# Kernel tuning notes

Hardware: AMD Instinct MI355X
Metric: run time of the kernel (lower is better)

## Reference

```python
import jax, jax.numpy as jnp
import numpy as np

EPS = 1e-6  # T5LayerNorm epsilon


def setup_inputs() -> dict:
    key = jax.random.key(0)
    k0, k1, k2, k3 = jax.random.split(key, 4)
    B, S, D, F, E = 4, 2048, 768, 3072, 8
    hidden_states = jax.random.normal(k0, (B, S, D), jnp.float32)
    router_w = jax.random.normal(k1, (E, D), jnp.float32) * 0.02
    ln_w = jnp.ones((E, D), jnp.float32)
    wi = jax.random.normal(k2, (E, F, D), jnp.float32) * 0.02
    wo = jax.random.normal(k3, (E, D, F), jnp.float32) * 0.02
    return {"hidden_states": hidden_states, "router_w": router_w, "ln_w": ln_w,
            "wi": wi, "wo": wo, "top_k": 2}


def reference(hidden_states, router_w, ln_w, wi, wo, top_k):
    B, S, D = hidden_states.shape
    E = router_w.shape[0]
    x = hidden_states.reshape(-1, D)                      # [T, D] tokens
    router_logits = x @ router_w.T                        # [T, E]
    probs = jax.nn.softmax(router_logits, axis=-1)
    rw, sel = jax.lax.top_k(probs, top_k)                 # [T, K]
    rw = rw / jnp.sum(rw, axis=-1, keepdims=True)         # renormalize top-k weights

    # T5LayerNorm is RMS-norm (no mean subtraction); shared input x, per-expert scale.
    var = jnp.mean(x * x, axis=-1, keepdims=True)         # [T, 1]
    x_norm = x * jax.lax.rsqrt(var + EPS)                 # [T, D]

    out = jnp.zeros_like(x)
    for e in range(E):  # fixed small loop over experts (structurally distinct params)
        # combine weight for expert e: zero for tokens that did not select it
        w_e = jnp.sum(jnp.where(sel == e, rw, 0.0), axis=-1)   # [T]
        h = x_norm * ln_w[e]                                   # [T, D]
        ff = jax.nn.relu(h @ wi[e].T) @ wo[e].T                # [T, D]
        # T5LayerFF returns x + FFN(LN(x)); routing weight scales the whole output
        out = out + w_e[:, None] * (x + ff)
    layer_output = out.reshape(B, S, D)
    return layer_output, router_logits
```

## Files before the change

kernel.cpp:

```cpp
#include <hip/hip_runtime.h>
#include <hip/hip_bf16.h>
#include <math.h>

typedef short short8 __attribute__((ext_vector_type(8)));
typedef float f32x16 __attribute__((ext_vector_type(16)));

constexpr int D = 768;
constexpr int E = 8;
constexpr int F = 3072;
constexpr int FH = 1536;
constexpr int T = 8192;
constexpr float EPS = 1e-6f;

static __device__ inline unsigned short f2bf(float f) {
    __hip_bfloat16 h = __float2bfloat16(f);
    return *reinterpret_cast<unsigned short*>(&h);
}

static __device__ inline f32x16 mfma_bf16(short8 a, short8 b, f32x16 c) {
    return __builtin_amdgcn_mfma_f32_32x32x16_bf16(a, b, c, 0, 0, 0);
}

#define GLL16(g, s) __builtin_amdgcn_global_load_lds( \
    (const __attribute__((address_space(1))) unsigned int*)(g), \
    (__attribute__((address_space(3))) unsigned int*)(s), 16, 0, 0)

__global__ __launch_bounds__(256)
void convert_weights(const float* __restrict__ wi, const float* __restrict__ wo,
                     const float* __restrict__ lnw,
                     unsigned short* __restrict__ wip, unsigned short* __restrict__ wop)
{
    const unsigned NWI = (unsigned)E * F * D;
    unsigned i4 = (blockIdx.x * 256u + threadIdx.x) * 4u;
    if (i4 < NWI) {
        float4 v = *(const float4*)(wi + i4);
        unsigned e = i4 / (unsigned)(F * D);
        unsigned d = i4 % (unsigned)D;
        float4 l = *(const float4*)(lnw + e * D + d);
        ushort4 o = { f2bf(v.x * l.x), f2bf(v.y * l.y), f2bf(v.z * l.z), f2bf(v.w * l.w) };
        *(ushort4*)(wip + i4) = o;
    } else {
        unsigned j = i4 - NWI;
        float4 v = *(const float4*)(wo + j);
        ushort4 o = { f2bf(v.x), f2bf(v.y), f2bf(v.z), f2bf(v.w) };
        *(ushort4*)(wop + j) = o;
    }
}

__global__ __launch_bounds__(256)
void router_norm_kernel(const float* __restrict__ x,
                        const float* __restrict__ rw,
                        float* __restrict__ logits,
                        unsigned short* __restrict__ xn,
                        float* __restrict__ out,
                        int*   __restrict__ sel,
                        float2* __restrict__ w01)
{
    const int lane = threadIdx.x & 63;
    const int wid  = threadIdx.x >> 6;
    const int t = blockIdx.x * 4 + wid;
    if (t >= T) return;

    const float* xr = x + (size_t)t * D;
    float xv[12];
    float acc[8];
#pragma unroll
    for (int e = 0; e < 8; ++e) acc[e] = 0.f;
    float ssq = 0.f;
#pragma unroll
    for (int i = 0; i < 12; ++i) {
        const int k = lane + 64 * i;
        const float v = xr[k];
        xv[i] = v;
        ssq += v * v;
#pragma unroll
        for (int e = 0; e < 8; ++e) acc[e] += v * rw[e * D + k];
    }
#pragma unroll
    for (int off = 32; off; off >>= 1) {
        ssq += __shfl_xor(ssq, off);
#pragma unroll
        for (int e = 0; e < 8; ++e) acc[e] += __shfl_xor(acc[e], off);
    }

    int e0 = 0; float m0 = acc[0];
#pragma unroll
    for (int e = 1; e < 8; ++e) if (acc[e] > m0) { m0 = acc[e]; e0 = e; }
    int e1 = -1; float m1 = -3.4e38f;
#pragma unroll
    for (int e = 0; e < 8; ++e) if (e != e0 && acc[e] > m1) { m1 = acc[e]; e1 = e; }

    const float r  = expf(m1 - m0);
    const float w0 = 1.f / (1.f + r);
    const float w1 = r * w0;
    const float wsum = w0 + w1;
    const float rs = rsqrtf(ssq * (1.f / (float)D) + EPS);

    if (lane == 0) {
#pragma unroll
        for (int e = 0; e < 8; ++e) logits[t * 8 + e] = acc[e];
        sel[t] = e0 | (e1 << 4);
        w01[t] = make_float2(w0, w1);
    }

#pragma unroll
    for (int i = 0; i < 12; ++i) {
        const int k = lane + 64 * i;
        xn[(size_t)t * D + k] = f2bf(xv[i] * rs);
        out[(size_t)t * D + k] = wsum * xv[i];
    }
}

__global__ __launch_bounds__(256)
void build_lists(const int* __restrict__ sel, const float2* __restrict__ w01,
                 int* __restrict__ counts, int* __restrict__ lists,
                 float* __restrict__ wlist)
{
    const int e = blockIdx.x;
    const int tid = threadIdx.x;
    const int lane = tid & 63;
    const int wv = tid >> 6;
    __shared__ int wtot[4];
    int cnt = 0;
    for (int c0 = 0; c0 < T; c0 += 256) {
        const int t = c0 + tid;
        const int s = sel[t];
        const bool m1 = ((s >> 4) & 15) == e;
        const bool m = ((s & 15) == e) || m1;
        const unsigned long long b = __ballot(m);
        const int pre = __popcll(b & ((1ULL << lane) - 1ULL));
        if (lane == 0) wtot[wv] = __popcll(b);
        __syncthreads();
        int wbase = 0;
#pragma unroll
        for (int i = 0; i < 4; ++i) if (i < wv) wbase += wtot[i];
        if (m) {
            const int pos = cnt + wbase + pre;
            lists[e * T + pos] = (t << 1) | (m1 ? 1 : 0);
            const float2 w = w01[t];
            wlist[e * T + pos] = m1 ? w.y : w.x;
        }
        cnt += wtot[0] + wtot[1] + wtot[2] + wtot[3];
        __syncthreads();
    }
    if (tid == 0) counts[e] = cnt;
}

__global__ __launch_bounds__(256)
void gemm1_kernel(const unsigned short* __restrict__ xn,
                  const unsigned short* __restrict__ wip,
                  const int* __restrict__ counts,
                  const int* __restrict__ lists,
                  unsigned short* __restrict__ H, int half)
{
    __shared__ __align__(16) char smem[65536];
    __shared__ int s_tok[128];

    const int bid = blockIdx.x;
    const int e  = bid & 7;
    const int mt = (bid >> 3) / 12;
    const int nt = (bid >> 3) % 12;
    const int cnt = counts[e];
    const int base = mt * 128;
    if (base >= cnt) return;
    int offe = 0;
    for (int i = 0; i < e; ++i) offe += counts[i];

    const int tid = threadIdx.x;
    const int w = tid >> 6, l = tid & 63;
    const int lo = l & 31, hi = l >> 5;
    const int wr = w >> 1, wc = w & 1;

    if (tid < 128) {
        const int idx = base + tid;
        s_tok[tid] = (idx < cnt) ? (lists[e * T + idx] >> 1) : 0;
    }
    __syncthreads();

    const int r = (w * 4 + 0) * 8 + (l >> 3);
    const int chS = ((l & 7) ^ ((l >> 3) & 7)) * 8;
    const unsigned short* aSrc[4];
    const unsigned short* bSrc[4];
#pragma unroll
    for (int j = 0; j < 4; ++j) {
        const int rj = r + j * 8;
        aSrc[j] = xn + (size_t)s_tok[rj] * D + chS;
        bSrc[j] = wip + ((size_t)e * F + half * FH + nt * 128 + rj) * D + chS;
    }

    f32x16 acc00, acc01, acc10, acc11;
#pragma unroll
    for (int q = 0; q < 16; ++q) { acc00[q] = 0.f; acc01[q] = 0.f; acc10[q] = 0.f; acc11[q] = 0.f; }

    const int rx = (lo & 7) << 4;
    const int arow0 = (wr * 64 + lo) * 128;
    const int arow1 = arow0 + 32 * 128;
    const int brow0 = (wc * 64 + lo) * 128;
    const int brow1 = brow0 + 32 * 128;
    const int stgOff = w * 4096;

#pragma unroll
    for (int j = 0; j < 4; ++j) {
        GLL16(aSrc[j], smem + stgOff + j * 1024);
        GLL16(bSrc[j], smem + 16384 + stgOff + j * 1024);
    }
    __syncthreads();

    int cur = 0;
    for (int kt = 0; kt < 12; ++kt) {
        const char* bufA = smem + (cur ^ 1) * 32768;
        if (kt < 11) {
            const int k1 = (kt + 1) * 64;
#pragma unroll
            for (int j = 0; j < 4; ++j) {
                GLL16(aSrc[j] + k1, bufA + stgOff + j * 1024);
                GLL16(bSrc[j] + k1, bufA + 16384 + stgOff + j * 1024);
            }
        }
        const char* cA = smem + cur * 32768;
        const char* cB = cA + 16384;
#pragma unroll
        for (int ks = 0; ks < 4; ++ks) {
            const int coff = (hi * 16 + ks * 32) ^ rx;
            short8 a0 = *(const short8*)(cA + arow0 + coff);
            short8 a1 = *(const short8*)(cA + arow1 + coff);
            short8 b0 = *(const short8*)(cB + brow0 + coff);
            short8 b1 = *(const short8*)(cB + brow1 + coff);
            acc00 = mfma_bf16(a0, b0, acc00);
            acc01 = mfma_bf16(a0, b1, acc01);
            acc10 = mfma_bf16(a1, b0, acc10);
            acc11 = mfma_bf16(a1, b1, acc11);
        }
        __syncthreads();
        cur ^= 1;
    }

    const int cbase = nt * 128 + wc * 64 + lo;
#pragma unroll
    for (int rr = 0; rr < 16; ++rr) {
        const int crow = (rr & 3) + 8 * (rr >> 2) + 4 * hi;
        int lrow = wr * 64 + crow;
        if (base + lrow < cnt) {
            unsigned short* hp = H + (size_t)(offe + base + lrow) * FH + cbase;
            hp[0]  = f2bf(fmaxf(acc00[rr], 0.f));
            hp[32] = f2bf(fmaxf(acc01[rr], 0.f));
        }
        lrow += 32;
        if (base + lrow < cnt) {
            unsigned short* hp = H + (size_t)(offe + base + lrow) * FH + cbase;
            hp[0]  = f2bf(fmaxf(acc10[rr], 0.f));
            hp[32] = f2bf(fmaxf(acc11[rr], 0.f));
        }
    }
}

__global__ __launch_bounds__(256)
void gemm2_kernel(const unsigned short* __restrict__ H,
                  const unsigned short* __restrict__ wop,
                  const int* __restrict__ counts,
                  const int* __restrict__ lists, const float* __restrict__ wlist,
                  float* __restrict__ out, int half)
{
    __shared__ __align__(16) char smem[65536];
    __shared__ int   s_tok[128];
    __shared__ float s_wgt[128];

    const int bid = blockIdx.x;
    const int e  = bid & 7;
    const int mt = (bid >> 3) / 6;
    const int nt = (bid >> 3) % 6;
    const int cnt = counts[e];
    const int base = mt * 128;
    if (base >= cnt) return;
    int offe = 0;
    for (int i = 0; i < e; ++i) offe += counts[i];

    const int tid = threadIdx.x;
    const int w = tid >> 6, l = tid & 63;
    const int lo = l & 31, hi = l >> 5;
    const int wr = w >> 1, wc = w & 1;

    if (tid < 128) {
        const int idx = base + tid;
        const bool v = idx < cnt;
        s_tok[tid] = v ? lists[e * T + idx] : 0;
        s_wgt[tid] = v ? wlist[e * T + idx] : 0.f;
    }

    const int r = (w * 4 + 0) * 8 + (l >> 3);
    const int chS = ((l & 7) ^ ((l >> 3) & 7)) * 8;
    const unsigned short* aSrc[4];
    const unsigned short* bSrc[4];
#pragma unroll
    for (int j = 0; j < 4; ++j) {
        const int rj = r + j * 8;
        aSrc[j] = H + (size_t)(offe + base + rj) * FH + chS;
        bSrc[j] = wop + ((size_t)e * D + nt * 128 + rj) * F + half * FH + chS;
    }

    f32x16 acc00, acc01, acc10, acc11;
#pragma unroll
    for (int q = 0; q < 16; ++q) { acc00[q] = 0.f; acc01[q] = 0.f; acc10[q] = 0.f; acc11[q] = 0.f; }

    const int rx = (lo & 7) << 4;
    const int arow0 = (wr * 64 + lo) * 128;
    const int arow1 = arow0 + 32 * 128;
    const int brow0 = (wc * 64 + lo) * 128;
    const int brow1 = brow0 + 32 * 128;
    const int stgOff = w * 4096;

#pragma unroll
    for (int j = 0; j < 4; ++j) {
        GLL16(aSrc[j], smem + stgOff + j * 1024);
        GLL16(bSrc[j], smem + 16384 + stgOff + j * 1024);
    }
    __syncthreads();

    int cur = 0;
    for (int kt = 0; kt < 24; ++kt) {
        const char* bufA = smem + (cur ^ 1) * 32768;
        if (kt < 23) {
            const int k1 = (kt + 1) * 64;
#pragma unroll
            for (int j = 0; j < 4; ++j) {
                GLL16(aSrc[j] + k1, bufA + stgOff + j * 1024);
                GLL16(bSrc[j] + k1, bufA + 16384 + stgOff + j * 1024);
            }
        }
        const char* cA = smem + cur * 32768;
        const char* cB = cA + 16384;
#pragma unroll
        for (int ks = 0; ks < 4; ++ks) {
            const int coff = (hi * 16 + ks * 32) ^ rx;
            short8 a0 = *(const short8*)(cA + arow0 + coff);
            short8 a1 = *(const short8*)(cA + arow1 + coff);
            short8 b0 = *(const short8*)(cB + brow0 + coff);
            short8 b1 = *(const short8*)(cB + brow1 + coff);
            acc00 = mfma_bf16(a0, b0, acc00);
            acc01 = mfma_bf16(a0, b1, acc01);
            acc10 = mfma_bf16(a1, b0, acc10);
            acc11 = mfma_bf16(a1, b1, acc11);
        }
        __syncthreads();
        cur ^= 1;
    }

    const int cbase = nt * 128 + wc * 64 + lo;
#pragma unroll
    for (int rr = 0; rr < 16; ++rr) {
        const int crow = (rr & 3) + 8 * (rr >> 2) + 4 * hi;
        int lrow = wr * 64 + crow;
        if (base + lrow < cnt) {
            const int tk = s_tok[lrow] >> 1;
            const float wgt = s_wgt[lrow];
            float* dst = out + (size_t)tk * D + cbase;
            atomicAdd(dst,      wgt * acc00[rr]);
            atomicAdd(dst + 32, wgt * acc01[rr]);
        }
        lrow += 32;
        if (base + lrow < cnt) {
            const int tk = s_tok[lrow] >> 1;
            const float wgt = s_wgt[lrow];
            float* dst = out + (size_t)tk * D + cbase;
            atomicAdd(dst,      wgt * acc10[rr]);
            atomicAdd(dst + 32, wgt * acc11[rr]);
        }
    }
}

extern "C" void kernel_launch(void* const* d_in, const int* in_sizes, int n_in,
                              void* d_out, int out_size, void* d_ws, size_t ws_size,
                              hipStream_t stream) {
    const float* x   = (const float*)d_in[0];
    const float* rw  = (const float*)d_in[1];
    const float* lnw = (const float*)d_in[2];
    const float* wi  = (const float*)d_in[3];
    const float* wo  = (const float*)d_in[4];

    float* out    = (float*)d_out;
    float* logits = (float*)d_out + (size_t)T * D;

    char* ws = (char*)d_ws;
    int*            counts = (int*)(ws);
    int*            sel    = (int*)(ws + 4096);
    float2*         w01    = (float2*)(ws + 65536);
    int*            lists  = (int*)(ws + 131072);
    float*          wlist  = (float*)(ws + 393216);
    unsigned short* xn     = (unsigned short*)(ws + 1048576);
    unsigned short* wip    = (unsigned short*)(ws + 13631488);
    unsigned short* wop    = (unsigned short*)(ws + 51380224);
    unsigned short* H      = (unsigned short*)(ws + 89128960);

    convert_weights<<<36864, 256, 0, stream>>>(wi, wo, lnw, wip, wop);

    router_norm_kernel<<<T / 4, 256, 0, stream>>>(x, rw, logits, xn, out,
                                                  sel, w01);

    build_lists<<<E, 256, 0, stream>>>(sel, w01, counts, lists, wlist);

    for (int h = 0; h < 2; ++h) {
        gemm1_kernel<<<32 * 12 * 8, 256, 0, stream>>>(xn, wip, counts,
                                                      lists, H, h);
        gemm2_kernel<<<32 * 6 * 8, 256, 0, stream>>>(H, wop, counts,
                                                     lists, wlist, out, h);
    }
}
```

Baseline: 375.8 us.

## Replace atomic scatter with per-slot ff buffer plus combine; single-buffer LDS

The gemm2 epilogue now writes (first half) or accumulates (second half) weighted results into a separate buffer indexed by token and top-k slot, instead of issuing float atomicAdds into the output. A new combine kernel then adds both slot buffers into the output. This path only runs when the workspace is large enough. Both GEMMs also drop the double-buffered global-to-LDS prefetch and use one 32 KB stage loaded each k-step before a barrier, which removes load/compute overlap but may allow more resident blocks. The change trades atomic traffic for extra plain stores and an extra elementwise pass.

After: 363.9 us. 1.03x faster.

```diff
diff --git a/kernel.cpp b/kernel.cpp
--- a/kernel.cpp
+++ b/kernel.cpp
@@ -153,7 +153,8 @@
                   const int* __restrict__ lists,
                   unsigned short* __restrict__ H, int half)
 {
-    __shared__ __align__(16) char smem[65536];
+    __shared__ unsigned short sA[128 * 64];
+    __shared__ unsigned short sB[128 * 64];
     __shared__ int s_tok[128];
 
     const int bid = blockIdx.x;
@@ -187,6 +188,8 @@
         aSrc[j] = xn + (size_t)s_tok[rj] * D + chS;
         bSrc[j] = wip + ((size_t)e * F + half * FH + nt * 128 + rj) * D + chS;
     }
+    char* sAc = (char*)sA;
+    char* sBc = (char*)sB;
 
     f32x16 acc00, acc01, acc10, acc11;
 #pragma unroll
@@ -197,42 +200,28 @@
     const int arow1 = arow0 + 32 * 128;
     const int brow0 = (wc * 64 + lo) * 128;
     const int brow1 = brow0 + 32 * 128;
-    const int stgOff = w * 4096;
-
-#pragma unroll
-    for (int j = 0; j < 4; ++j) {
-        GLL16(aSrc[j], smem + stgOff + j * 1024);
-        GLL16(bSrc[j], smem + 16384 + stgOff + j * 1024);
-    }
-    __syncthreads();
-
-    int cur = 0;
+
     for (int kt = 0; kt < 12; ++kt) {
-        const char* bufA = smem + (cur ^ 1) * 32768;
-        if (kt < 11) {
-            const int k1 = (kt + 1) * 64;
-#pragma unroll
-            for (int j = 0; j < 4; ++j) {
-                GLL16(aSrc[j] + k1, bufA + stgOff + j * 1024);
-                GLL16(bSrc[j] + k1, bufA + 16384 + stgOff + j * 1024);
-            }
-        }
-        const char* cA = smem + cur * 32768;
-        const char* cB = cA + 16384;
+        const int k0 = kt * 64;
+#pragma unroll
+        for (int j = 0; j < 4; ++j) {
+            GLL16(aSrc[j] + k0, sAc + (w * 4 + j) * 1024);
+            GLL16(bSrc[j] + k0, sBc + (w * 4 + j) * 1024);
+        }
+        __syncthreads();
 #pragma unroll
         for (int ks = 0; ks < 4; ++ks) {
             const int coff = (hi * 16 + ks * 32) ^ rx;
-            short8 a0 = *(const short8*)(cA + arow0 + coff);
-            short8 a1 = *(const short8*)(cA + arow1 + coff);
-            short8 b0 = *(const short8*)(cB + brow0 + coff);
-            short8 b1 = *(const short8*)(cB + brow1 + coff);
+            short8 a0 = *(const short8*)(sAc + arow0 + coff);
+            short8 a1 = *(const short8*)(sAc + arow1 + coff);
+            short8 b0 = *(const short8*)(sBc + brow0 + coff);
+            short8 b1 = *(const short8*)(sBc + brow1 + coff);
             acc00 = mfma_bf16(a0, b0, acc00);
             acc01 = mfma_bf16(a0, b1, acc01);
             acc10 = mfma_bf16(a1, b0, acc10);
             acc11 = mfma_bf16(a1, b1, acc11);
         }
         __syncthreads();
-        cur ^= 1;
     }
 
     const int cbase = nt * 128 + wc * 64 + lo;
@@ -259,9 +248,11 @@
                   const unsigned short* __restrict__ wop,
                   const int* __restrict__ counts,
                   const int* __restrict__ lists, const float* __restrict__ wlist,
-                  float* __restrict__ out, int half)
-{
-    __shared__ __align__(16) char smem[65536];
+                  float* __restrict__ out, float* __restrict__ ffout,
+                  int half, int mode)
+{
+    __shared__ unsigned short sA[128 * 64];
+    __shared__ unsigned short sB[128 * 64];
     __shared__ int   s_tok[128];
     __shared__ float s_wgt[128];
 
@@ -297,6 +288,8 @@
         aSrc[j] = H + (size_t)(offe + base + rj) * FH + chS;
         bSrc[j] = wop + ((size_t)e * D + nt * 128 + rj) * F + half * FH + chS;
     }
+    char* sAc = (char*)sA;
+    char* sBc = (char*)sB;
 
     f32x16 acc00, acc01, acc10, acc11;
 #pragma unroll
@@ -307,65 +300,66 @@
     const int arow1 = arow0 + 32 * 128;
     const int brow0 = (wc * 64 + lo) * 128;
     const int brow1 = brow0 + 32 * 128;
-    const int stgOff = w * 4096;
-
-#pragma unroll
-    for (int j = 0; j < 4; ++j) {
-        GLL16(aSrc[j], smem + stgOff + j * 1024);
-        GLL16(bSrc[j], smem + 16384 + stgOff + j * 1024);
-    }
-    __syncthreads();
-
-    int cur = 0;
+
     for (int kt = 0; kt < 24; ++kt) {
-        const char* bufA = smem + (cur ^ 1) * 32768;
-        if (kt < 23) {
-            const int k1 = (kt + 1) * 64;
-#pragma unroll
-            for (int j = 0; j < 4; ++j) {
-                GLL16(aSrc[j] + k1, bufA + stgOff + j * 1024);
-                GLL16(bSrc[j] + k1, bufA + 16384 + stgOff + j * 1024);
-            }
-        }
-        const char* cA = smem + cur * 32768;
-        const char* cB = cA + 16384;
+        const int k0 = kt * 64;
+#pragma unroll
+        for (int j = 0; j < 4; ++j) {
+            GLL16(aSrc[j] + k0, sAc + (w * 4 + j) * 1024);
+            GLL16(bSrc[j] + k0, sBc + (w * 4 + j) * 1024);
+        }
+        __syncthreads();
 #pragma unroll
         for (int ks = 0; ks < 4; ++ks) {
             const int coff = (hi * 16 + ks * 32) ^ rx;
-            short8 a0 = *(const short8*)(cA + arow0 + coff);
-            short8 a1 = *(const short8*)(cA + arow1 + coff);
-            short8 b0 = *(const short8*)(cB + brow0 + coff);
-            short8 b1 = *(const short8*)(cB + brow1 + coff);
+            short8 a0 = *(const short8*)(sAc + arow0 + coff);
+            short8 a1 = *(const short8*)(sAc + arow1 + coff);
+            short8 b0 = *(const short8*)(sBc + brow0 + coff);
+            short8 b1 = *(const short8*)(sBc + brow1 + coff);
             acc00 = mfma_bf16(a0, b0, acc00);
             acc01 = mfma_bf16(a0, b1, acc01);
             acc10 = mfma_bf16(a1, b0, acc10);
             acc11 = mfma_bf16(a1, b1, acc11);
         }
         __syncthreads();
-        cur ^= 1;
     }
 
     const int cbase = nt * 128 + wc * 64 + lo;
 #pragma unroll
     for (int rr = 0; rr < 16; ++rr) {
         const int crow = (rr & 3) + 8 * (rr >> 2) + 4 * hi;
-        int lrow = wr * 64 + crow;
-        if (base + lrow < cnt) {
-            const int tk = s_tok[lrow] >> 1;
-            const float wgt = s_wgt[lrow];
-            float* dst = out + (size_t)tk * D + cbase;
-            atomicAdd(dst,      wgt * acc00[rr]);
-            atomicAdd(dst + 32, wgt * acc01[rr]);
-        }
-        lrow += 32;
-        if (base + lrow < cnt) {
-            const int tk = s_tok[lrow] >> 1;
-            const float wgt = s_wgt[lrow];
-            float* dst = out + (size_t)tk * D + cbase;
-            atomicAdd(dst,      wgt * acc10[rr]);
-            atomicAdd(dst + 32, wgt * acc11[rr]);
-        }
-    }
+#pragma unroll
+        for (int mh = 0; mh < 2; ++mh) {
+            const int lrow = wr * 64 + crow + mh * 32;
+            if (base + lrow < cnt) {
+                const int pk = s_tok[lrow];
+                const float wgt = s_wgt[lrow];
+                const float v0 = wgt * (mh ? acc10[rr] : acc00[rr]);
+                const float v1 = wgt * (mh ? acc11[rr] : acc01[rr]);
+                if (mode == 0) {
+                    float* dst = out + (size_t)(pk >> 1) * D + cbase;
+                    atomicAdd(dst,      v0);
+                    atomicAdd(dst + 32, v1);
+                } else {
+                    float* dst = ffout + ((size_t)(pk & 1) * T + (pk >> 1)) * D + cbase;
+                    if (mode == 1) { dst[0] = v0;  dst[32] = v1; }
+                    else           { dst[0] += v0; dst[32] += v1; }
+                }
+            }
+        }
+    }
+}
+
+__global__ __launch_bounds__(256)
+void combine_kernel(const float* __restrict__ ffout, float* __restrict__ out)
+{
+    const long long i4 = ((long long)blockIdx.x * 256 + threadIdx.x) * 4;
+    float4 o  = *(const float4*)(out + i4);
+    float4 f0 = *(const float4*)(ffout + i4);
+    float4 f1 = *(const float4*)(ffout + (long long)T * D + i4);
+    o.x += f0.x + f1.x; o.y += f0.y + f1.y;
+    o.z += f0.z + f1.z; o.w += f0.w + f1.w;
+    *(float4*)(out + i4) = o;
 }
 
 extern "C" void kernel_launch(void* const* d_in, const int* in_sizes, int n_in,
@@ -390,6 +384,9 @@
     unsigned short* wip    = (unsigned short*)(ws + 13631488);
     unsigned short* wop    = (unsigned short*)(ws + 51380224);
     unsigned short* H      = (unsigned short*)(ws + 89128960);
+    float*          ffout  = (float*)(ws + 140247040);
+
+    const bool big = ws_size >= 190578688ULL;
 
     convert_weights<<<36864, 256, 0, stream>>>(wi, wo, lnw, wip, wop);
 
@@ -401,7 +398,11 @@
     for (int h = 0; h < 2; ++h) {
         gemm1_kernel<<<32 * 12 * 8, 256, 0, stream>>>(xn, wip, counts,
                                                       lists, H, h);
+        const int mode = big ? (h ? 2 : 1) : 0;
         gemm2_kernel<<<32 * 6 * 8, 256, 0, stream>>>(H, wop, counts,
-                                                     lists, wlist, out, h);
-    }
-}
+                                                     lists, wlist, out,
+                                                     ffout, h, mode);
+    }
+
+    if (big) combine_kernel<<<T * D / 4 / 256, 256, 0, stream>>>(ffout, out);
+}
```
